# Kernel tuning notes

Hardware: AMD Instinct MI355X
Metric: run time of the kernel (lower is better)

Reference implementation:

```python
import jax, jax.numpy as jnp
import numpy as np

B, F, R, L, P = 16384, 64, 1024, 4, 128  # batch, features, rules, max conditions, interaction pairs


def setup_inputs() -> dict:
    key = jax.random.key(0)
    ks = jax.random.split(key, 8)
    x = jax.random.normal(ks[0], (B, F), dtype=jnp.float32)
    attention_weights = jax.random.uniform(ks[1], (F,), dtype=jnp.float32, minval=0.5, maxval=1.5)
    premise_params = jnp.ones((R,), dtype=jnp.float32)
    rule_threshs = jax.random.normal(ks[2], (R, L), dtype=jnp.float32)
    # signs are +/-1 (split direction of each XGBoost condition)
    rule_signs = jnp.where(jax.random.randint(ks[3], (R, L), 0, 2) == 1, 1.0, -1.0).astype(jnp.float32)
    rule_masks = (jax.random.uniform(ks[4], (R, L)) < 0.9).astype(jnp.float32)
    rule_masks = rule_masks.at[:, 0].set(1.0)
    consequent_params = jax.random.normal(ks[5], (R, 1 + F + F + P), dtype=jnp.float32) * 0.01
    rule_feat_idxs = jax.random.randint(ks[6], (R, L), 0, F)
    interaction_pairs = jax.random.randint(ks[7], (P, 2), 0, F)
    return {
        "x": x,
        "attention_weights": attention_weights,
        "premise_params": premise_params,
        "rule_threshs": rule_threshs,
        "rule_signs": rule_signs,
        "rule_masks": rule_masks,
        "consequent_params": consequent_params,
        "rule_feat_idxs": rule_feat_idxs,
        "interaction_pairs": interaction_pairs,
    }


def reference(x, attention_weights, premise_params, rule_threshs, rule_signs,
              rule_masks, consequent_params, rule_feat_idxs, interaction_pairs):
    # attention scaling
    x_att = x * attention_weights  # [B, F]

    # --- fuzzify_and_infer ---
    sel = x_att[:, rule_feat_idxs]  # gather -> [B, R, L]
    z = premise_params[None, :, None] * (sel - rule_threshs[None]) * rule_signs[None]
    mf = jax.nn.sigmoid(z)
    masked_mf = mf * rule_masks[None] + (1.0 - rule_masks[None])  # inactive conds -> 1
    firing = jnp.prod(masked_mf, axis=2)  # [B, R]
    w = firing / (jnp.sum(firing, axis=1, keepdims=True) + 1e-8)  # normalized firing

    # --- TSK polynomials (order=2 with interactions): [x, x^2, xi*xj, 1] ---
    inter = x_att[:, interaction_pairs[:, 0]] * x_att[:, interaction_pairs[:, 1]]  # [B, P]
    ones = jnp.ones((x.shape[0], 1), dtype=x.dtype)
    p = jnp.concatenate([x_att, x_att * x_att, inter, ones], axis=1)  # [B, 1+2F+P]

    # weighted consequent sum: y_b = sum_r w_br * (p_b . theta_r)
    y = jnp.einsum('br,bi,ri->b', w, p, consequent_params)
    return y
```

## Files before the change

### kernel.cpp

```cpp
#include <hip/hip_runtime.h>

typedef short short8 __attribute__((ext_vector_type(8)));
typedef float f32x4 __attribute__((ext_vector_type(4)));

#define KP 288

#define OFF_CP   0ULL
#define OFF_A2   589824ULL
#define OFF_C2   606208ULL
#define OFF_IX   622592ULL
#define OFF_PAIR 626688ULL
#define OFF_NUM  626944ULL
#define OFF_DEN  692480ULL

__device__ __forceinline__ unsigned short f2bf(float f) {
  unsigned u = __float_as_uint(f);
  return (unsigned short)((u + 0x7FFFu + ((u >> 16) & 1u)) >> 16);
}

__global__ __launch_bounds__(256) void prep_kernel(
    const float* __restrict__ pp, const float* __restrict__ th,
    const float* __restrict__ sg, const float* __restrict__ mk,
    const float* __restrict__ cp, const int* __restrict__ fidx,
    const int* __restrict__ pairs, unsigned char* __restrict__ ws)
{
  unsigned short* cp_out = (unsigned short*)(ws + OFF_CP);
  float* a2o = (float*)(ws + OFF_A2);
  float* c2o = (float*)(ws + OFF_C2);
  unsigned* ixo = (unsigned*)(ws + OFF_IX);
  unsigned short* pro = (unsigned short*)(ws + OFF_PAIR);
  int bid = blockIdx.x, t = threadIdx.x;

  if (bid < 288) {
    int e = bid * 1024 + t * 4;
#pragma unroll
    for (int q = 0; q < 4; ++q, ++e) {
      int r = e / KP, c = e - r * KP;
      cp_out[e] = f2bf(c < 257 ? cp[r * 257 + c] : 0.f);
    }
  } else if (bid < 292) {
    int r = (bid - 288) * 256 + t;
    float p = pp[r];
    unsigned pk = 0;
#pragma unroll
    for (int l = 0; l < 4; ++l) {
      float m = mk[r * 4 + l], s = sg[r * 4 + l], tt = th[r * 4 + l];
      float A, C;
      if (m != 0.f) { A = -1.44269504f * p * s; C = 1.44269504f * p * s * tt; }
      else          { A = 0.f;                  C = -126.f; }
      a2o[r * 4 + l] = A; c2o[r * 4 + l] = C;
      pk |= ((unsigned)fidx[r * 4 + l] & 0xFFu) << (8 * l);
    }
    ixo[r] = pk;
  } else if (bid == 292) {
    if (t < 128)
      pro[t] = (unsigned short)((pairs[2 * t] & 0xFF) | ((pairs[2 * t + 1] & 0xFF) << 8));
  } else {
    float* dst = (float*)(ws + (bid == 293 ? OFF_NUM : OFF_DEN));
#pragma unroll
    for (int q = 0; q < 64; ++q) dst[q * 256 + t] = 0.f;
  }
}

__global__ __launch_bounds__(256, 4) void main_kernel(
    const unsigned char* __restrict__ ws,
    const float* __restrict__ x, const float* __restrict__ att,
    float* __restrict__ numg, float* __restrict__ deng)
{
  __shared__ float xa[64 * 68];
  __shared__ short lCP[256 * 32];
  __shared__ short lP[64 * 32];
  __shared__ unsigned short lPair[128];

  const unsigned short* CP = (const unsigned short*)(ws + OFF_CP);
  const float4* A2p = (const float4*)(ws + OFF_A2);
  const float4* C2p = (const float4*)(ws + OFF_C2);
  const unsigned* IX = (const unsigned*)(ws + OFF_IX);
  const unsigned short* PRW = (const unsigned short*)(ws + OFF_PAIR);

  int t = threadIdx.x, l = t & 63, w = t >> 6;
  int g = l >> 4, lr = l & 15;
  int b0 = blockIdx.x * 64, r0 = blockIdx.y * 256;

  if (t < 128) lPair[t] = PRW[t];
  {
#pragma unroll
    for (int i = 0; i < 4; ++i) {
      int idx = t + i * 256, row = idx >> 4, c4 = idx & 15;
      float4 a4 = ((const float4*)att)[c4];
      float4 v = ((const float4*)(x + (size_t)(b0 + row) * 64))[c4];
      v.x *= a4.x; v.y *= a4.y; v.z *= a4.z; v.w *= a4.w;
      *(float4*)&xa[row * 68 + c4 * 4] = v;
    }
  }
  __syncthreads();

  f32x4 acc[4][4];
#pragma unroll
  for (int mi = 0; mi < 4; ++mi)
#pragma unroll
    for (int ni = 0; ni < 4; ++ni)
      acc[mi][ni] = (f32x4){0.f, 0.f, 0.f, 0.f};

  int row2 = t >> 2, q = t & 3;
  int sw2 = (row2 ^ (row2 >> 2)) & 3;
  const float* xr2 = &xa[row2 * 68];

#pragma unroll
  for (int ks = 0; ks < 9; ++ks) {
    int k0 = ks * 32;
    short8 cpr[4];
#pragma unroll
    for (int i = 0; i < 4; ++i) {
      int rowc = row2 + i * 64;
      cpr[i] = *(const short8*)(CP + (size_t)(r0 + rowc) * KP + k0 + q * 8);
    }
    short8 vp;
    int fb = k0 + q * 8;
    if (fb < 64) {
      float4 u0 = *(const float4*)&xr2[fb], u1 = *(const float4*)&xr2[fb + 4];
      vp[0] = f2bf(u0.x); vp[1] = f2bf(u0.y); vp[2] = f2bf(u0.z); vp[3] = f2bf(u0.w);
      vp[4] = f2bf(u1.x); vp[5] = f2bf(u1.y); vp[6] = f2bf(u1.z); vp[7] = f2bf(u1.w);
    } else if (fb < 128) {
      float4 u0 = *(const float4*)&xr2[fb - 64], u1 = *(const float4*)&xr2[fb - 60];
      vp[0] = f2bf(u0.x * u0.x); vp[1] = f2bf(u0.y * u0.y);
      vp[2] = f2bf(u0.z * u0.z); vp[3] = f2bf(u0.w * u0.w);
      vp[4] = f2bf(u1.x * u1.x); vp[5] = f2bf(u1.y * u1.y);
      vp[6] = f2bf(u1.z * u1.z); vp[7] = f2bf(u1.w * u1.w);
    } else if (fb < 256) {
      const unsigned* pw = (const unsigned*)&lPair[fb - 128];
#pragma unroll
      for (int u = 0; u < 4; ++u) {
        unsigned pk = pw[u];
        vp[2 * u]     = f2bf(xr2[pk & 255] * xr2[(pk >> 8) & 255]);
        vp[2 * u + 1] = f2bf(xr2[(pk >> 16) & 255] * xr2[pk >> 24]);
      }
    } else {
#pragma unroll
      for (int j = 0; j < 8; ++j) vp[j] = (fb + j == 256) ? (short)0x3F80 : (short)0;
    }
    __syncthreads();
#pragma unroll
    for (int i = 0; i < 4; ++i) {
      int rowc = row2 + i * 64;
      int swc = (rowc ^ (rowc >> 2)) & 3;
      *(short8*)&lCP[rowc * 32 + ((q ^ swc) * 8)] = cpr[i];
    }
    *(short8*)&lP[row2 * 32 + ((q ^ sw2) * 8)] = vp;
    __syncthreads();
    short8 aF[4], bF[4];
#pragma unroll
    for (int mi = 0; mi < 4; ++mi) {
      int row = w * 64 + mi * 16 + lr;
      int s = (row ^ (row >> 2)) & 3;
      aF[mi] = *(const short8*)&lCP[row * 32 + ((g ^ s) * 8)];
    }
#pragma unroll
    for (int ni = 0; ni < 4; ++ni) {
      int row = ni * 16 + lr;
      int s = (row ^ (row >> 2)) & 3;
      bF[ni] = *(const short8*)&lP[row * 32 + ((g ^ s) * 8)];
    }
#pragma unroll
    for (int mi = 0; mi < 4; ++mi)
#pragma unroll
      for (int ni = 0; ni < 4; ++ni)
        acc[mi][ni] = __builtin_amdgcn_mfma_f32_16x16x32_bf16(aF[mi], bF[ni], acc[mi][ni], 0, 0, 0);
  }

  float num[4] = {0.f, 0.f, 0.f, 0.f}, den[4] = {0.f, 0.f, 0.f, 0.f};
#pragma unroll
  for (int mi = 0; mi < 4; ++mi) {
#pragma unroll
    for (int j = 0; j < 4; ++j) {
      int rule = r0 + w * 64 + mi * 16 + (g << 2) + j;
      float4 A2 = A2p[rule], C2 = C2p[rule];
      unsigned pk = IX[rule];
      int f0 = pk & 255, f1 = (pk >> 8) & 255, f2 = (pk >> 16) & 255, f3 = pk >> 24;
#pragma unroll
      for (int ni = 0; ni < 4; ++ni) {
        const float* xr = &xa[(ni * 16 + lr) * 68];
        float D = 1.f;
        float e0 = exp2f(fmaf(A2.x, xr[f0], C2.x)); D = fmaf(D, e0, D);
        float e1 = exp2f(fmaf(A2.y, xr[f1], C2.y)); D = fmaf(D, e1, D);
        float e2 = exp2f(fmaf(A2.z, xr[f2], C2.z)); D = fmaf(D, e2, D);
        float e3 = exp2f(fmaf(A2.w, xr[f3], C2.w)); D = fmaf(D, e3, D);
        float fir = __builtin_amdgcn_rcpf(D);
        num[ni] = fmaf(fir, acc[mi][ni][j], num[ni]);
        den[ni] += fir;
      }
    }
  }

#pragma unroll
  for (int ni = 0; ni < 4; ++ni) {
    float n = num[ni], d = den[ni];
    n += __shfl_xor(n, 16, 64); n += __shfl_xor(n, 32, 64);
    d += __shfl_xor(d, 16, 64); d += __shfl_xor(d, 32, 64);
    num[ni] = n; den[ni] = d;
  }
  float nv = 0.f, dv = 0.f;
#pragma unroll
  for (int ni = 0; ni < 4; ++ni)
    if (g == ni) { nv = num[ni]; dv = den[ni]; }
  atomicAdd(&numg[b0 + (g << 4) + lr], nv);
  atomicAdd(&deng[b0 + (g << 4) + lr], dv);
}

__global__ __launch_bounds__(256) void fin_kernel(
    const float* __restrict__ numg, const float* __restrict__ deng,
    float* __restrict__ y)
{
  int i = blockIdx.x * 256 + threadIdx.x;
  y[i] = numg[i] / (deng[i] + 1e-8f);
}

extern "C" void kernel_launch(void* const* d_in, const int* in_sizes, int n_in,
                              void* d_out, int out_size, void* d_ws, size_t ws_size,
                              hipStream_t stream) {
  (void)in_sizes; (void)n_in; (void)out_size; (void)ws_size;
  const float* x    = (const float*)d_in[0];
  const float* att  = (const float*)d_in[1];
  const float* pp   = (const float*)d_in[2];
  const float* th   = (const float*)d_in[3];
  const float* sg   = (const float*)d_in[4];
  const float* mk   = (const float*)d_in[5];
  const float* cp   = (const float*)d_in[6];
  const int* fidx   = (const int*)d_in[7];
  const int* pairs  = (const int*)d_in[8];
  unsigned char* ws = (unsigned char*)d_ws;
  float* numg = (float*)(ws + OFF_NUM);
  float* deng = (float*)(ws + OFF_DEN);

  prep_kernel<<<295, 256, 0, stream>>>(pp, th, sg, mk, cp, fidx, pairs, ws);
  main_kernel<<<dim3(256, 4), 256, 0, stream>>>(ws, x, att, numg, deng);
  fin_kernel<<<64, 256, 0, stream>>>(numg, deng, (float*)d_out);
}
```

Baseline: 118.9 us.

## Prefetch next K-slice of consequent params and pad x tile to stride 65

Global loads of the next 32-column slice of bf16 consequent params are now issued before the barrier, so they overlap the MFMA work of the current slice. The x_att shared tile stride changes from 68 to 65 to cut bank conflicts on the gathered per-feature reads, which forces scalar stores in place of float4. The ks loop is no longer unrolled, A fragments are loaded one at a time to save registers, and launch bounds drop from 4 to 3 waves per SIMD. The lower occupancy hint and the scalar LDS accesses could offset the gain from the prefetch.

New measurement: 104.5 us. -12.1%, faster.

```diff
diff --git a/kernel.cpp b/kernel.cpp
--- a/kernel.cpp
+++ b/kernel.cpp
@@ -12,6 +12,8 @@
 #define OFF_PAIR 626688ULL
 #define OFF_NUM  626944ULL
 #define OFF_DEN  692480ULL
+
+#define XS 65
 
 __device__ __forceinline__ unsigned short f2bf(float f) {
   unsigned u = __float_as_uint(f);
@@ -62,12 +64,12 @@
   }
 }
 
-__global__ __launch_bounds__(256, 4) void main_kernel(
+__global__ __launch_bounds__(256, 3) void main_kernel(
     const unsigned char* __restrict__ ws,
     const float* __restrict__ x, const float* __restrict__ att,
     float* __restrict__ numg, float* __restrict__ deng)
 {
-  __shared__ float xa[64 * 68];
+  __shared__ float xa[64 * XS];
   __shared__ short lCP[256 * 32];
   __shared__ short lP[64 * 32];
   __shared__ unsigned short lPair[128];
@@ -89,8 +91,9 @@
       int idx = t + i * 256, row = idx >> 4, c4 = idx & 15;
       float4 a4 = ((const float4*)att)[c4];
       float4 v = ((const float4*)(x + (size_t)(b0 + row) * 64))[c4];
-      v.x *= a4.x; v.y *= a4.y; v.z *= a4.z; v.w *= a4.w;
-      *(float4*)&xa[row * 68 + c4 * 4] = v;
+      float* dst = &xa[row * XS + c4 * 4];
+      dst[0] = v.x * a4.x; dst[1] = v.y * a4.y;
+      dst[2] = v.z * a4.z; dst[3] = v.w * a4.w;
     }
   }
   __syncthreads();
@@ -104,30 +107,24 @@
 
   int row2 = t >> 2, q = t & 3;
   int sw2 = (row2 ^ (row2 >> 2)) & 3;
-  const float* xr2 = &xa[row2 * 68];
-
-#pragma unroll
+  const float* xr2 = &xa[row2 * XS];
+
+  short8 cpr[4];
+#pragma unroll
+  for (int i = 0; i < 4; ++i)
+    cpr[i] = *(const short8*)(CP + (size_t)(r0 + row2 + i * 64) * KP + q * 8);
+
   for (int ks = 0; ks < 9; ++ks) {
     int k0 = ks * 32;
-    short8 cpr[4];
-#pragma unroll
-    for (int i = 0; i < 4; ++i) {
-      int rowc = row2 + i * 64;
-      cpr[i] = *(const short8*)(CP + (size_t)(r0 + rowc) * KP + k0 + q * 8);
-    }
+    int fb = k0 + q * 8;
     short8 vp;
-    int fb = k0 + q * 8;
-    if (fb < 64) {
-      float4 u0 = *(const float4*)&xr2[fb], u1 = *(const float4*)&xr2[fb + 4];
-      vp[0] = f2bf(u0.x); vp[1] = f2bf(u0.y); vp[2] = f2bf(u0.z); vp[3] = f2bf(u0.w);
-      vp[4] = f2bf(u1.x); vp[5] = f2bf(u1.y); vp[6] = f2bf(u1.z); vp[7] = f2bf(u1.w);
-    } else if (fb < 128) {
-      float4 u0 = *(const float4*)&xr2[fb - 64], u1 = *(const float4*)&xr2[fb - 60];
-      vp[0] = f2bf(u0.x * u0.x); vp[1] = f2bf(u0.y * u0.y);
-      vp[2] = f2bf(u0.z * u0.z); vp[3] = f2bf(u0.w * u0.w);
-      vp[4] = f2bf(u1.x * u1.x); vp[5] = f2bf(u1.y * u1.y);
-      vp[6] = f2bf(u1.z * u1.z); vp[7] = f2bf(u1.w * u1.w);
-    } else if (fb < 256) {
+    if (ks < 2) {
+#pragma unroll
+      for (int j = 0; j < 8; ++j) vp[j] = f2bf(xr2[fb + j]);
+    } else if (ks < 4) {
+#pragma unroll
+      for (int j = 0; j < 8; ++j) { float u = xr2[fb - 64 + j]; vp[j] = f2bf(u * u); }
+    } else if (ks < 8) {
       const unsigned* pw = (const unsigned*)&lPair[fb - 128];
 #pragma unroll
       for (int u = 0; u < 4; ++u) {
@@ -147,14 +144,13 @@
       *(short8*)&lCP[rowc * 32 + ((q ^ swc) * 8)] = cpr[i];
     }
     *(short8*)&lP[row2 * 32 + ((q ^ sw2) * 8)] = vp;
+    if (ks < 8) {
+#pragma unroll
+      for (int i = 0; i < 4; ++i)
+        cpr[i] = *(const short8*)(CP + (size_t)(r0 + row2 + i * 64) * KP + k0 + 32 + q * 8);
+    }
     __syncthreads();
-    short8 aF[4], bF[4];
-#pragma unroll
-    for (int mi = 0; mi < 4; ++mi) {
-      int row = w * 64 + mi * 16 + lr;
-      int s = (row ^ (row >> 2)) & 3;
-      aF[mi] = *(const short8*)&lCP[row * 32 + ((g ^ s) * 8)];
-    }
+    short8 bF[4];
 #pragma unroll
     for (int ni = 0; ni < 4; ++ni) {
       int row = ni * 16 + lr;
@@ -162,10 +158,14 @@
       bF[ni] = *(const short8*)&lP[row * 32 + ((g ^ s) * 8)];
     }
 #pragma unroll
-    for (int mi = 0; mi < 4; ++mi)
+    for (int mi = 0; mi < 4; ++mi) {
+      int row = w * 64 + mi * 16 + lr;
+      int s = (row ^ (row >> 2)) & 3;
+      short8 aF = *(const short8*)&lCP[row * 32 + ((g ^ s) * 8)];
 #pragma unroll
       for (int ni = 0; ni < 4; ++ni)
-        acc[mi][ni] = __builtin_amdgcn_mfma_f32_16x16x32_bf16(aF[mi], bF[ni], acc[mi][ni], 0, 0, 0);
+        acc[mi][ni] = __builtin_amdgcn_mfma_f32_16x16x32_bf16(aF, bF[ni], acc[mi][ni], 0, 0, 0);
+    }
   }
 
   float num[4] = {0.f, 0.f, 0.f, 0.f}, den[4] = {0.f, 0.f, 0.f, 0.f};
@@ -179,7 +179,7 @@
       int f0 = pk & 255, f1 = (pk >> 8) & 255, f2 = (pk >> 16) & 255, f3 = pk >> 24;
 #pragma unroll
       for (int ni = 0; ni < 4; ++ni) {
-        const float* xr = &xa[(ni * 16 + lr) * 68];
+        const float* xr = &xa[(ni * 16 + lr) * XS];
         float D = 1.f;
         float e0 = exp2f(fmaf(A2.x, xr[f0], C2.x)); D = fmaf(D, e0, D);
         float e1 = exp2f(fmaf(A2.y, xr[f1], C2.y)); D = fmaf(D, e1, D);
```
